# Kernel optimization log

Hardware: AMD Instinct MI355X
Metric: run time of the kernel (lower is better)

## Reference

```python
import jax, jax.numpy as jnp
import numpy as np

N = 100000      # nodes
E = 1600000     # edges
F_IN = 64       # node_features
F_OUT = 32      # output_size


def _cheb2(H, row, col, w_norm, theta, bias):
    # ChebConv K=2, sym normalization, lambda_max=2 (GCLSTM default):
    # L_hat = L - I = -D^{-1/2} A D^{-1/2}, so T0 = H, T1 = -A_norm H
    agg = jax.ops.segment_sum(w_norm[:, None] * H[col], row, num_segments=N)  # [N, F_OUT]
    return H @ theta[0] - agg @ theta[1] + bias


def setup_inputs() -> dict:
    key = jax.random.key(0)
    ks = jax.random.split(key, 24)
    inp = {}
    inp["x"] = jax.random.normal(ks[0], (N, F_IN), jnp.float32)
    inp["edge_index"] = jax.random.randint(ks[1], (2, E), 0, N)
    inp["edge_weight"] = jax.random.uniform(ks[2], (E,), jnp.float32)
    inp["h"] = jax.random.normal(ks[3], (N, F_OUT), jnp.float32)
    inp["c"] = jax.random.normal(ks[4], (N, F_OUT), jnp.float32)
    s_in = float(1.0 / np.sqrt(F_IN))
    s_out = float(1.0 / np.sqrt(F_OUT))
    i = 5
    for g in "ifco":
        inp[f"W_{g}"] = jax.random.uniform(ks[i], (F_IN, F_OUT), jnp.float32, -s_in, s_in); i += 1
        inp[f"b_{g}"] = jax.random.uniform(ks[i], (1, F_OUT), jnp.float32, -s_in, s_in); i += 1
        inp[f"theta_{g}"] = jax.random.uniform(ks[i], (2, F_OUT, F_OUT), jnp.float32, -s_out, s_out); i += 1
        inp[f"cb_{g}"] = jax.random.uniform(ks[i], (F_OUT,), jnp.float32, -s_out, s_out); i += 1
    inp["W_lin"] = jax.random.uniform(ks[i], (F_OUT, 1), jnp.float32, -s_out, s_out); i += 1
    inp["b_lin"] = jax.random.uniform(ks[i], (1,), jnp.float32, -s_out, s_out)
    return inp


def reference(x, edge_index, edge_weight, h, c,
              W_i, b_i, theta_i, cb_i,
              W_f, b_f, theta_f, cb_f,
              W_c, b_c, theta_c, cb_c,
              W_o, b_o, theta_o, cb_o,
              W_lin, b_lin):
    row, col = edge_index[0], edge_index[1]
    # symmetric normalization of edge weights (get_laplacian 'sym')
    deg = jax.ops.segment_sum(edge_weight, row, num_segments=N)
    dis = jnp.where(deg > 0, jax.lax.rsqrt(jnp.where(deg > 0, deg, 1.0)), 0.0)
    w_norm = dis[row] * edge_weight * dis[col]  # [E]
    # GCLSTM gates: input x through dense W, hidden h through ChebConv
    I = jax.nn.sigmoid(x @ W_i + _cheb2(h, row, col, w_norm, theta_i, cb_i) + b_i)
    Fg = jax.nn.sigmoid(x @ W_f + _cheb2(h, row, col, w_norm, theta_f, cb_f) + b_f)
    T = jnp.tanh(x @ W_c + _cheb2(h, row, col, w_norm, theta_c, cb_c) + b_c)
    C = Fg * c + I * T
    O = jax.nn.sigmoid(x @ W_o + _cheb2(h, row, col, w_norm, theta_o, cb_o) + b_o)
    H = O * jnp.tanh(C)
    # wrapper head: relu then Linear(out, 1)
    return jax.nn.relu(H) @ W_lin + b_lin  # [N, 1]
```

## Files before the change

### kernel.cpp

```cpp
#include <hip/hip_runtime.h>
#include <math.h>

#define NN 100000
#define NE 1600000
#define EPB 8192
#define NEB 196
#define NBUK 391
#define CAP 8192

#define DEGSCALE 16777216.0f

typedef __attribute__((ext_vector_type(8))) short bf16x8;
typedef __attribute__((ext_vector_type(4))) float f32x4;

#define MFMA(A, B, C) __builtin_amdgcn_mfma_f32_16x16x32_bf16(A, B, C, 0, 0, 0)

__device__ __forceinline__ float sigm(float z) { return 1.0f / (1.0f + expf(-z)); }

__device__ __forceinline__ void split1(float v, unsigned short* hi, unsigned short* lo) {
  unsigned u = __float_as_uint(v);
  *hi = (unsigned short)(u >> 16);
  float hf = __uint_as_float(u & 0xFFFF0000u);
  float lf = v - hf;
  *lo = (unsigned short)(__float_as_uint(lf) >> 16);
}

__device__ __forceinline__ void split8(const float* f, bf16x8* hi, bf16x8* lo) {
#pragma unroll
  for (int j = 0; j < 8; ++j) {
    unsigned short h, l;
    split1(f[j], &h, &l);
    (*hi)[j] = (short)h;
    (*lo)[j] = (short)l;
  }
}

__device__ __forceinline__ bf16x8 as_bf16x8(uint4 q) {
  union { uint4 q; bf16x8 v; } u;
  u.q = q;
  return u.v;
}

__device__ __forceinline__ void load8(const float4* p, int idx4, float* f) {
  float4 a = p[idx4];
  float4 b = p[idx4 + 1];
  f[0] = a.x; f[1] = a.y; f[2] = a.z; f[3] = a.w;
  f[4] = b.x; f[5] = b.y; f[6] = b.z; f[7] = b.w;
}


__global__ __launch_bounds__(256) void k_p1(const int* __restrict__ row,
                                            int* __restrict__ counts) {
  __shared__ int hist[NBUK];
  for (int i = threadIdx.x; i < NBUK; i += 256) hist[i] = 0;
  __syncthreads();
  int e0 = blockIdx.x * EPB;
  int e1 = min(e0 + EPB, NE);
  for (int e = e0 + (int)threadIdx.x; e < e1; e += 256)
    atomicAdd(&hist[row[e] >> 8], 1);
  __syncthreads();
  for (int i = threadIdx.x; i < NBUK; i += 256)
    counts[blockIdx.x * NBUK + i] = hist[i];
}

__global__ __launch_bounds__(256) void k_s1(int* __restrict__ counts,
                                            int* __restrict__ total) {
  __shared__ int s[256];
  int b = blockIdx.x;
  int t = threadIdx.x;
  int v = (t < NEB) ? counts[t * NBUK + b] : 0;
  s[t] = v;
  __syncthreads();
  for (int o = 1; o < 256; o <<= 1) {
    int a = (t >= o) ? s[t - o] : 0;
    __syncthreads();
    s[t] += a;
    __syncthreads();
  }
  if (t < NEB) counts[t * NBUK + b] = s[t] - v;
  if (t == 255) total[b] = s[255];
}

struct S2PParams {
  const int* total;
  int* bases;
  const float* W[4];
  const float* T0[4];
  const float* T1[4];
  const float* b[4];
  const float* cb[4];
  uint4* fh;
  uint4* fl;
  float* bias;
};

__global__ __launch_bounds__(512) void k_s2p(S2PParams pp) {
  if (blockIdx.x == 0) {
    __shared__ int s[512];
    int t = threadIdx.x;
    int v = (t < NBUK) ? pp.total[t] : 0;
    s[t] = v;
    __syncthreads();
    for (int o = 1; o < 512; o <<= 1) {
      int a = (t >= o) ? s[t - o] : 0;
      __syncthreads();
      s[t] += a;
      __syncthreads();
    }
    if (t < NBUK) pp.bases[t] = s[t] - v;
    if (t == 0) pp.bases[NBUK] = NE;
    return;
  }
  int idx = (blockIdx.x - 1) * 512 + threadIdx.x;
  if (idx < 2048) {
    int T = idx >> 6;
    int lane = idx & 63;
    int ncol = ((T & 7) * 16) + (lane & 15);
    int g = ncol >> 5;
    int c = ncol & 31;
    int kq = (lane >> 4) * 8;
    const float* mat;
    int kbase;
    if (T < 16) { mat = pp.W[g]; kbase = (T >> 3) * 32 + kq; }
    else if (T < 24) { mat = pp.T0[g]; kbase = kq; }
    else { mat = pp.T1[g]; kbase = kq; }
    unsigned hw[4], lw[4];
#pragma unroll
    for (int jj = 0; jj < 4; ++jj) {
      unsigned short h0, l0, h1, l1;
      split1(mat[(kbase + 2 * jj) * 32 + c], &h0, &l0);
      split1(mat[(kbase + 2 * jj + 1) * 32 + c], &h1, &l1);
      hw[jj] = (unsigned)h0 | ((unsigned)h1 << 16);
      lw[jj] = (unsigned)l0 | ((unsigned)l1 << 16);
    }
    pp.fh[idx] = make_uint4(hw[0], hw[1], hw[2], hw[3]);
    pp.fl[idx] = make_uint4(lw[0], lw[1], lw[2], lw[3]);
  }
  if (blockIdx.x == 1 && threadIdx.x < 128) {
    int g = threadIdx.x >> 5;
    int c = threadIdx.x & 31;
    pp.bias[threadIdx.x] = pp.b[g][c] + pp.cb[g][c];
  }
}

__global__ __launch_bounds__(256) void k_p2(const int* __restrict__ row,
                                            const int* __restrict__ col,
                                            const float* __restrict__ ew,
                                            const int* __restrict__ rel,
                                            const int* __restrict__ bases,
                                            int2* __restrict__ colw) {
  __shared__ int cursor[NBUK];
  for (int i = threadIdx.x; i < NBUK; i += 256)
    cursor[i] = bases[i] + rel[blockIdx.x * NBUK + i];
  __syncthreads();
  int e0 = blockIdx.x * EPB;
  int e1 = min(e0 + EPB, NE);
  for (int e = e0 + (int)threadIdx.x; e < e1; e += 256) {
    int r = row[e];
    int c = col[e];
    float w = ew[e];
    int slot = atomicAdd(&cursor[r >> 8], 1);
    colw[slot] = make_int2(c | ((r & 255) << 17), __float_as_int(w));
  }
}

__global__ __launch_bounds__(256) void k_bucket(const int* __restrict__ bases,
                                               int2* __restrict__ colw,
                                               int* __restrict__ rowptr,
                                               float* __restrict__ dis) {
  __shared__ int2 stage[CAP];
  __shared__ int cnt[256], degfx[256], s[256], cursor[256];
  int b = blockIdx.x;
  int base = bases[b];
  int M = bases[b + 1] - base;
  if (M > CAP) M = CAP;
  int t = threadIdx.x;
  cnt[t] = 0;
  degfx[t] = 0;
  __syncthreads();
  for (int i = t; i < M; i += 256) {
    int2 e = colw[base + i];
    stage[i] = e;
    int rl = (e.x >> 17) & 255;
    atomicAdd(&cnt[rl], 1);
    unsigned fx = (unsigned)(__int_as_float(e.y) * DEGSCALE + 0.5f);
    atomicAdd((unsigned*)&degfx[rl], fx);
  }
  __syncthreads();
  int v = cnt[t];
  s[t] = v;
  __syncthreads();
  for (int o = 1; o < 256; o <<= 1) {
    int a = (t >= o) ? s[t - o] : 0;
    __syncthreads();
    s[t] += a;
    __syncthreads();
  }
  int excl = s[t] - v;
  int node = b * 256 + t;
  if (node <= NN) rowptr[node] = base + excl;
  if (node < NN) {
    unsigned fx = (unsigned)degfx[t];
    dis[node] = fx ? rsqrtf((float)fx * (1.0f / DEGSCALE)) : 0.0f;
  }
  cursor[t] = excl;
  __syncthreads();
  for (int i = t; i < M; i += 256) {
    int2 e = stage[i];
    int rl = (e.x >> 17) & 255;
    int r = atomicAdd(&cursor[rl], 1);
    colw[base + r] = e;
  }
}

struct FusedParams {
  const float4* x4;
  const float4* h4;
  const float* cst;
  const int* rowptr;
  const int2* colw;
  const float* dis;
  const uint4* fh;
  const uint4* fl;
  const float* bias;
  const float* wlin;
  const float* blin;
  float* out;
};

__global__ __launch_bounds__(256) void k_fused(FusedParams p) {
  const int lane = threadIdx.x & 63;
  const int wv = threadIdx.x >> 6;
  const int m0 = blockIdx.x * 64 + wv * 16;
  const int mr = lane & 15;
  const int quad = lane >> 4;
  int m = m0 + mr;
  if (m >= NN) m = NN - 1;

  bf16x8 xh[2], xl[2], hh, hl, gh, gl;
  float f[8];
#pragma unroll
  for (int kt = 0; kt < 2; ++kt) {
    load8(p.x4, (m * 64 + kt * 32 + quad * 8) >> 2, f);
    split8(f, &xh[kt], &xl[kt]);
  }
  load8(p.h4, (m * 32 + quad * 8) >> 2, f);
  split8(f, &hh, &hl);

  float fa[8] = {0.f, 0.f, 0.f, 0.f, 0.f, 0.f, 0.f, 0.f};
  float fb[8] = {0.f, 0.f, 0.f, 0.f, 0.f, 0.f, 0.f, 0.f};
  {
    int s0 = p.rowptr[m];
    int s1v = p.rowptr[m + 1];
    int j = s0;
    for (; j + 1 < s1v; j += 2) {
      int2 cw0 = p.colw[j];
      int2 cw1 = p.colw[j + 1];
      int c0 = cw0.x & 0x1FFFF;
      int c1 = cw1.x & 0x1FFFF;
      float w0 = __int_as_float(cw0.y) * p.dis[c0];
      float w1 = __int_as_float(cw1.y) * p.dis[c1];
      const float4* hp0 = p.h4 + c0 * 8 + quad * 2;
      const float4* hp1 = p.h4 + c1 * 8 + quad * 2;
      float4 a0 = hp0[0], a1 = hp0[1];
      float4 b0 = hp1[0], b1 = hp1[1];
      fa[0] = fmaf(w0, a0.x, fa[0]); fa[1] = fmaf(w0, a0.y, fa[1]);
      fa[2] = fmaf(w0, a0.z, fa[2]); fa[3] = fmaf(w0, a0.w, fa[3]);
      fa[4] = fmaf(w0, a1.x, fa[4]); fa[5] = fmaf(w0, a1.y, fa[5]);
      fa[6] = fmaf(w0, a1.z, fa[6]); fa[7] = fmaf(w0, a1.w, fa[7]);
      fb[0] = fmaf(w1, b0.x, fb[0]); fb[1] = fmaf(w1, b0.y, fb[1]);
      fb[2] = fmaf(w1, b0.z, fb[2]); fb[3] = fmaf(w1, b0.w, fb[3]);
      fb[4] = fmaf(w1, b1.x, fb[4]); fb[5] = fmaf(w1, b1.y, fb[5]);
      fb[6] = fmaf(w1, b1.z, fb[6]); fb[7] = fmaf(w1, b1.w, fb[7]);
    }
    if (j < s1v) {
      int2 cw0 = p.colw[j];
      int c0 = cw0.x & 0x1FFFF;
      float w0 = __int_as_float(cw0.y) * p.dis[c0];
      const float4* hp0 = p.h4 + c0 * 8 + quad * 2;
      float4 a0 = hp0[0], a1 = hp0[1];
      fa[0] = fmaf(w0, a0.x, fa[0]); fa[1] = fmaf(w0, a0.y, fa[1]);
      fa[2] = fmaf(w0, a0.z, fa[2]); fa[3] = fmaf(w0, a0.w, fa[3]);
      fa[4] = fmaf(w0, a1.x, fa[4]); fa[5] = fmaf(w0, a1.y, fa[5]);
      fa[6] = fmaf(w0, a1.z, fa[6]); fa[7] = fmaf(w0, a1.w, fa[7]);
    }
  }
  {
    float dn = -p.dis[m];
#pragma unroll
    for (int j = 0; j < 8; ++j) f[j] = dn * (fa[j] + fb[j]);
    split8(f, &gh, &gl);
  }

  float wl0 = p.wlin[mr];
  float wl1 = p.wlin[mr + 16];
  float bl = p.blin[0];

  f32x4 acc[8];
#pragma unroll 2
  for (int nt = 0; nt < 8; ++nt) {
    float bv = p.bias[nt * 16 + mr];
    f32x4 a;
    a[0] = bv; a[1] = bv; a[2] = bv; a[3] = bv;
    bf16x8 b0h = as_bf16x8(p.fh[nt * 64 + lane]);
    bf16x8 b0l = as_bf16x8(p.fl[nt * 64 + lane]);
    bf16x8 b1h = as_bf16x8(p.fh[(8 + nt) * 64 + lane]);
    bf16x8 b1l = as_bf16x8(p.fl[(8 + nt) * 64 + lane]);
    bf16x8 t0h = as_bf16x8(p.fh[(16 + nt) * 64 + lane]);
    bf16x8 t0l = as_bf16x8(p.fl[(16 + nt) * 64 + lane]);
    bf16x8 t1h = as_bf16x8(p.fh[(24 + nt) * 64 + lane]);
    bf16x8 t1l = as_bf16x8(p.fl[(24 + nt) * 64 + lane]);
    a = MFMA(xh[0], b0h, a); a = MFMA(xh[0], b0l, a); a = MFMA(xl[0], b0h, a);
    a = MFMA(xh[1], b1h, a); a = MFMA(xh[1], b1l, a); a = MFMA(xl[1], b1h, a);
    a = MFMA(hh, t0h, a);    a = MFMA(hh, t0l, a);    a = MFMA(hl, t0h, a);
    a = MFMA(gh, t1h, a);    a = MFMA(gh, t1l, a);    a = MFMA(gl, t1h, a);
    acc[nt] = a;
  }

#pragma unroll
  for (int r = 0; r < 4; ++r) {
    int node = m0 + quad * 4 + r;
    int nc = node < NN ? node : NN - 1;
    float c0 = p.cst[nc * 32 + mr];
    float c1 = p.cst[nc * 32 + 16 + mr];
    float I0 = sigm(acc[0][r]), I1 = sigm(acc[1][r]);
    float F0 = sigm(acc[2][r]), F1 = sigm(acc[3][r]);
    float T0 = tanhf(acc[4][r]), T1 = tanhf(acc[5][r]);
    float O0 = sigm(acc[6][r]), O1 = sigm(acc[7][r]);
    float C0 = fmaf(F0, c0, I0 * T0);
    float C1 = fmaf(F1, c1, I1 * T1);
    float H0 = O0 * tanhf(C0);
    float H1 = O1 * tanhf(C1);
    float part = fmaf(fmaxf(H0, 0.f), wl0, fmaxf(H1, 0.f) * wl1);
#pragma unroll
    for (int s = 1; s < 16; s <<= 1) part += __shfl_xor(part, s, 64);
    if (mr == 0 && node < NN) p.out[node] = part + bl;
  }
}

extern "C" void kernel_launch(void* const* d_in, const int* in_sizes, int n_in,
                              void* d_out, int out_size, void* d_ws, size_t ws_size,
                              hipStream_t stream) {
  const float* x = (const float*)d_in[0];
  const int* row = (const int*)d_in[1];
  const int* col = row + NE;
  const float* ew = (const float*)d_in[2];
  const float* h = (const float*)d_in[3];
  const float* c = (const float*)d_in[4];

  float* ws = (float*)d_ws;
  float* dis = ws;
  int* rowptr = (int*)(ws + 100000);
  int* counts = (int*)(ws + 200004);
  int* total = (int*)(ws + 276640);
  int* bases = (int*)(ws + 277032);
  uint4* fh = (uint4*)(ws + 277424);
  uint4* fl = (uint4*)(ws + 285616);
  float* biasws = ws + 293808;
  int2* colw = (int2*)(ws + 293936);

  k_p1<<<NEB, 256, 0, stream>>>(row, counts);
  k_s1<<<NBUK, 256, 0, stream>>>(counts, total);

  S2PParams sp;
  sp.total = total;
  sp.bases = bases;
  for (int g = 0; g < 4; ++g) {
    sp.W[g] = (const float*)d_in[5 + 4 * g];
    sp.b[g] = (const float*)d_in[6 + 4 * g];
    sp.T0[g] = (const float*)d_in[7 + 4 * g];
    sp.T1[g] = sp.T0[g] + 1024;
    sp.cb[g] = (const float*)d_in[8 + 4 * g];
  }
  sp.fh = fh;
  sp.fl = fl;
  sp.bias = biasws;
  k_s2p<<<9, 512, 0, stream>>>(sp);

  k_p2<<<NEB, 256, 0, stream>>>(row, col, ew, counts, bases, colw);
  k_bucket<<<NBUK, 256, 0, stream>>>(bases, colw, rowptr, dis);

  FusedParams fp;
  fp.x4 = (const float4*)x;
  fp.h4 = (const float4*)h;
  fp.cst = c;
  fp.rowptr = rowptr;
  fp.colw = colw;
  fp.dis = dis;
  fp.fh = fh;
  fp.fl = fl;
  fp.bias = biasws;
  fp.wlin = (const float*)d_in[21];
  fp.blin = (const float*)d_in[22];
  fp.out = (float*)d_out;
  k_fused<<<(NN + 63) / 64, 256, 0, stream>>>(fp);
}
```

Measured before the change: 242.9 us.

## Replace bucketed CSR build with global-atomic counting sort and prescaled weights

The shared-memory two-level bucket sort (per-block histograms, scans, bucket scatter, in-bucket reorder) is replaced by a per-row counting sort. Row counts and degrees come from global atomics, followed by a two-kernel prefix scan and an atomic-cursor scatter that writes column/weight pairs. The scatter pre-multiplies each edge weight by dis[col], so the fused kernel no longer gathers dis per edge. The aggregation loop is also software-pipelined to load the next four edges early. The cost is heavy global atomic traffic on 100k counters, including float atomics that make the degree sum order nondeterministic, plus scattered uncoalesced writes; workspace regions for deg and btot are reused by colw.

Result: slower. 441.2 us (+81.6%).

```diff
diff --git a/kernel.cpp b/kernel.cpp
--- a/kernel.cpp
+++ b/kernel.cpp
@@ -3,12 +3,8 @@
 
 #define NN 100000
 #define NE 1600000
-#define EPB 8192
-#define NEB 196
 #define NBUK 391
-#define CAP 8192
-
-#define DEGSCALE 16777216.0f
+#define NPAD (NBUK * 256)
 
 typedef __attribute__((ext_vector_type(8))) short bf16x8;
 typedef __attribute__((ext_vector_type(4))) float f32x4;
@@ -49,41 +45,9 @@
 }
 
 
-__global__ __launch_bounds__(256) void k_p1(const int* __restrict__ row,
-                                            int* __restrict__ counts) {
-  __shared__ int hist[NBUK];
-  for (int i = threadIdx.x; i < NBUK; i += 256) hist[i] = 0;
-  __syncthreads();
-  int e0 = blockIdx.x * EPB;
-  int e1 = min(e0 + EPB, NE);
-  for (int e = e0 + (int)threadIdx.x; e < e1; e += 256)
-    atomicAdd(&hist[row[e] >> 8], 1);
-  __syncthreads();
-  for (int i = threadIdx.x; i < NBUK; i += 256)
-    counts[blockIdx.x * NBUK + i] = hist[i];
-}
-
-__global__ __launch_bounds__(256) void k_s1(int* __restrict__ counts,
-                                            int* __restrict__ total) {
-  __shared__ int s[256];
-  int b = blockIdx.x;
-  int t = threadIdx.x;
-  int v = (t < NEB) ? counts[t * NBUK + b] : 0;
-  s[t] = v;
-  __syncthreads();
-  for (int o = 1; o < 256; o <<= 1) {
-    int a = (t >= o) ? s[t - o] : 0;
-    __syncthreads();
-    s[t] += a;
-    __syncthreads();
-  }
-  if (t < NEB) counts[t * NBUK + b] = s[t] - v;
-  if (t == 255) total[b] = s[255];
-}
-
-struct S2PParams {
-  const int* total;
-  int* bases;
+struct InitParams {
+  int* cnt;
+  float* deg;
   const float* W[4];
   const float* T0[4];
   const float* T1[4];
@@ -94,24 +58,13 @@
   float* bias;
 };
 
-__global__ __launch_bounds__(512) void k_s2p(S2PParams pp) {
-  if (blockIdx.x == 0) {
-    __shared__ int s[512];
-    int t = threadIdx.x;
-    int v = (t < NBUK) ? pp.total[t] : 0;
-    s[t] = v;
-    __syncthreads();
-    for (int o = 1; o < 512; o <<= 1) {
-      int a = (t >= o) ? s[t - o] : 0;
-      __syncthreads();
-      s[t] += a;
-      __syncthreads();
-    }
-    if (t < NBUK) pp.bases[t] = s[t] - v;
-    if (t == 0) pp.bases[NBUK] = NE;
-    return;
-  }
-  int idx = (blockIdx.x - 1) * 512 + threadIdx.x;
+__global__ __launch_bounds__(512) void k_init(InitParams pp) {
+  int idx = blockIdx.x * 512 + threadIdx.x;
+  int stride = gridDim.x * 512;
+  for (int i = idx; i < NPAD; i += stride) {
+    pp.cnt[i] = 0;
+    pp.deg[i] = 0.0f;
+  }
   if (idx < 2048) {
     int T = idx >> 6;
     int lane = idx & 63;
@@ -136,58 +89,36 @@
     pp.fh[idx] = make_uint4(hw[0], hw[1], hw[2], hw[3]);
     pp.fl[idx] = make_uint4(lw[0], lw[1], lw[2], lw[3]);
   }
-  if (blockIdx.x == 1 && threadIdx.x < 128) {
-    int g = threadIdx.x >> 5;
-    int c = threadIdx.x & 31;
-    pp.bias[threadIdx.x] = pp.b[g][c] + pp.cb[g][c];
-  }
-}
-
-__global__ __launch_bounds__(256) void k_p2(const int* __restrict__ row,
-                                            const int* __restrict__ col,
-                                            const float* __restrict__ ew,
-                                            const int* __restrict__ rel,
-                                            const int* __restrict__ bases,
-                                            int2* __restrict__ colw) {
-  __shared__ int cursor[NBUK];
-  for (int i = threadIdx.x; i < NBUK; i += 256)
-    cursor[i] = bases[i] + rel[blockIdx.x * NBUK + i];
-  __syncthreads();
-  int e0 = blockIdx.x * EPB;
-  int e1 = min(e0 + EPB, NE);
-  for (int e = e0 + (int)threadIdx.x; e < e1; e += 256) {
+  if (idx < 128) {
+    int g = idx >> 5;
+    int c = idx & 31;
+    pp.bias[idx] = pp.b[g][c] + pp.cb[g][c];
+  }
+}
+
+__global__ __launch_bounds__(256) void k_hist(const int* __restrict__ row,
+                                              const float* __restrict__ ew,
+                                              int* __restrict__ cnt,
+                                              float* __restrict__ deg) {
+  int stride = gridDim.x * 256;
+  for (int e = blockIdx.x * 256 + threadIdx.x; e < NE; e += stride) {
     int r = row[e];
-    int c = col[e];
-    float w = ew[e];
-    int slot = atomicAdd(&cursor[r >> 8], 1);
-    colw[slot] = make_int2(c | ((r & 255) << 17), __float_as_int(w));
-  }
-}
-
-__global__ __launch_bounds__(256) void k_bucket(const int* __restrict__ bases,
-                                               int2* __restrict__ colw,
-                                               int* __restrict__ rowptr,
-                                               float* __restrict__ dis) {
-  __shared__ int2 stage[CAP];
-  __shared__ int cnt[256], degfx[256], s[256], cursor[256];
+    atomicAdd(&cnt[r], 1);
+    atomicAdd(&deg[r], ew[e]);
+  }
+}
+
+__global__ __launch_bounds__(256) void k_scan_a(const float* __restrict__ deg,
+                                                float* __restrict__ dis,
+                                                int* __restrict__ cursor,
+                                                int* __restrict__ btot) {
+  __shared__ int s[256];
   int b = blockIdx.x;
-  int base = bases[b];
-  int M = bases[b + 1] - base;
-  if (M > CAP) M = CAP;
   int t = threadIdx.x;
-  cnt[t] = 0;
-  degfx[t] = 0;
-  __syncthreads();
-  for (int i = t; i < M; i += 256) {
-    int2 e = colw[base + i];
-    stage[i] = e;
-    int rl = (e.x >> 17) & 255;
-    atomicAdd(&cnt[rl], 1);
-    unsigned fx = (unsigned)(__int_as_float(e.y) * DEGSCALE + 0.5f);
-    atomicAdd((unsigned*)&degfx[rl], fx);
-  }
-  __syncthreads();
-  int v = cnt[t];
+  int n = b * 256 + t;
+  int v = cursor[n];
+  float dg = deg[n];
+  if (n < NN) dis[n] = dg > 0.0f ? rsqrtf(dg) : 0.0f;
   s[t] = v;
   __syncthreads();
   for (int o = 1; o < 256; o <<= 1) {
@@ -196,20 +127,39 @@
     s[t] += a;
     __syncthreads();
   }
-  int excl = s[t] - v;
-  int node = b * 256 + t;
-  if (node <= NN) rowptr[node] = base + excl;
-  if (node < NN) {
-    unsigned fx = (unsigned)degfx[t];
-    dis[node] = fx ? rsqrtf((float)fx * (1.0f / DEGSCALE)) : 0.0f;
-  }
-  cursor[t] = excl;
+  cursor[n] = s[t] - v;
+  if (t == 255) btot[b] = s[255];
+}
+
+__global__ __launch_bounds__(256) void k_scan_c(const int* __restrict__ btot,
+                                                int* __restrict__ cursor) {
+  __shared__ int s[256];
+  int b = blockIdx.x;
+  int t = threadIdx.x;
+  int acc = 0;
+  for (int j = t; j < b; j += 256) acc += btot[j];
+  s[t] = acc;
   __syncthreads();
-  for (int i = t; i < M; i += 256) {
-    int2 e = stage[i];
-    int rl = (e.x >> 17) & 255;
-    int r = atomicAdd(&cursor[rl], 1);
-    colw[base + r] = e;
+  for (int o = 128; o > 0; o >>= 1) {
+    if (t < o) s[t] += s[t + o];
+    __syncthreads();
+  }
+  cursor[b * 256 + t] += s[0];
+}
+
+__global__ __launch_bounds__(256) void k_scatter(const int* __restrict__ row,
+                                                 const int* __restrict__ col,
+                                                 const float* __restrict__ ew,
+                                                 const float* __restrict__ dis,
+                                                 int* __restrict__ cursor,
+                                                 int2* __restrict__ colw) {
+  int stride = gridDim.x * 256;
+  for (int e = blockIdx.x * 256 + threadIdx.x; e < NE; e += stride) {
+    int r = row[e];
+    int c = col[e];
+    float w = ew[e] * dis[c];
+    int slot = atomicAdd(&cursor[r], 1);
+    colw[slot] = make_int2(c, __float_as_int(w));
   }
 }
 
@@ -217,7 +167,7 @@
   const float4* x4;
   const float4* h4;
   const float* cst;
-  const int* rowptr;
+  const int* cursor;
   const int2* colw;
   const float* dis;
   const uint4* fh;
@@ -228,6 +178,17 @@
   float* out;
 };
 
+__device__ __forceinline__ void accrow(const FusedParams& p, int quad, int2 cw,
+                                       float* acc) {
+  const float4* hp = p.h4 + (cw.x * 8 + quad * 2);
+  float4 a0 = hp[0], a1 = hp[1];
+  float w = __int_as_float(cw.y);
+  acc[0] = fmaf(w, a0.x, acc[0]); acc[1] = fmaf(w, a0.y, acc[1]);
+  acc[2] = fmaf(w, a0.z, acc[2]); acc[3] = fmaf(w, a0.w, acc[3]);
+  acc[4] = fmaf(w, a1.x, acc[4]); acc[5] = fmaf(w, a1.y, acc[5]);
+  acc[6] = fmaf(w, a1.z, acc[6]); acc[7] = fmaf(w, a1.w, acc[7]);
+}
+
 __global__ __launch_bounds__(256) void k_fused(FusedParams p) {
   const int lane = threadIdx.x & 63;
   const int wv = threadIdx.x >> 6;
@@ -250,40 +211,48 @@
   float fa[8] = {0.f, 0.f, 0.f, 0.f, 0.f, 0.f, 0.f, 0.f};
   float fb[8] = {0.f, 0.f, 0.f, 0.f, 0.f, 0.f, 0.f, 0.f};
   {
-    int s0 = p.rowptr[m];
-    int s1v = p.rowptr[m + 1];
-    int j = s0;
-    for (; j + 1 < s1v; j += 2) {
-      int2 cw0 = p.colw[j];
-      int2 cw1 = p.colw[j + 1];
-      int c0 = cw0.x & 0x1FFFF;
-      int c1 = cw1.x & 0x1FFFF;
-      float w0 = __int_as_float(cw0.y) * p.dis[c0];
-      float w1 = __int_as_float(cw1.y) * p.dis[c1];
-      const float4* hp0 = p.h4 + c0 * 8 + quad * 2;
-      const float4* hp1 = p.h4 + c1 * 8 + quad * 2;
-      float4 a0 = hp0[0], a1 = hp0[1];
-      float4 b0 = hp1[0], b1 = hp1[1];
-      fa[0] = fmaf(w0, a0.x, fa[0]); fa[1] = fmaf(w0, a0.y, fa[1]);
-      fa[2] = fmaf(w0, a0.z, fa[2]); fa[3] = fmaf(w0, a0.w, fa[3]);
-      fa[4] = fmaf(w0, a1.x, fa[4]); fa[5] = fmaf(w0, a1.y, fa[5]);
-      fa[6] = fmaf(w0, a1.z, fa[6]); fa[7] = fmaf(w0, a1.w, fa[7]);
-      fb[0] = fmaf(w1, b0.x, fb[0]); fb[1] = fmaf(w1, b0.y, fb[1]);
-      fb[2] = fmaf(w1, b0.z, fb[2]); fb[3] = fmaf(w1, b0.w, fb[3]);
-      fb[4] = fmaf(w1, b1.x, fb[4]); fb[5] = fmaf(w1, b1.y, fb[5]);
-      fb[6] = fmaf(w1, b1.z, fb[6]); fb[7] = fmaf(w1, b1.w, fb[7]);
+    int end = p.cursor[m];
+    int s0 = (m == 0) ? 0 : p.cursor[m - 1];
+    int rem = end - s0;
+    const int2* ep = p.colw + s0;
+    int i = 0;
+    if (rem >= 4) {
+      int2 w0 = ep[0], w1 = ep[1], w2 = ep[2], w3 = ep[3];
+      for (i = 4; i + 3 < rem; i += 4) {
+        const float4* h0 = p.h4 + (w0.x * 8 + quad * 2);
+        const float4* h1 = p.h4 + (w1.x * 8 + quad * 2);
+        const float4* h2 = p.h4 + (w2.x * 8 + quad * 2);
+        const float4* h3 = p.h4 + (w3.x * 8 + quad * 2);
+        float4 a0 = h0[0], a1 = h0[1];
+        float4 b0 = h1[0], b1 = h1[1];
+        float4 c0 = h2[0], c1 = h2[1];
+        float4 d0 = h3[0], d1 = h3[1];
+        float f0 = __int_as_float(w0.y), f1 = __int_as_float(w1.y);
+        float f2 = __int_as_float(w2.y), f3 = __int_as_float(w3.y);
+        w0 = ep[i]; w1 = ep[i + 1]; w2 = ep[i + 2]; w3 = ep[i + 3];
+        fa[0] = fmaf(f0, a0.x, fa[0]); fa[1] = fmaf(f0, a0.y, fa[1]);
+        fa[2] = fmaf(f0, a0.z, fa[2]); fa[3] = fmaf(f0, a0.w, fa[3]);
+        fa[4] = fmaf(f0, a1.x, fa[4]); fa[5] = fmaf(f0, a1.y, fa[5]);
+        fa[6] = fmaf(f0, a1.z, fa[6]); fa[7] = fmaf(f0, a1.w, fa[7]);
+        fb[0] = fmaf(f1, b0.x, fb[0]); fb[1] = fmaf(f1, b0.y, fb[1]);
+        fb[2] = fmaf(f1, b0.z, fb[2]); fb[3] = fmaf(f1, b0.w, fb[3]);
+        fb[4] = fmaf(f1, b1.x, fb[4]); fb[5] = fmaf(f1, b1.y, fb[5]);
+        fb[6] = fmaf(f1, b1.z, fb[6]); fb[7] = fmaf(f1, b1.w, fb[7]);
+        fa[0] = fmaf(f2, c0.x, fa[0]); fa[1] = fmaf(f2, c0.y, fa[1]);
+        fa[2] = fmaf(f2, c0.z, fa[2]); fa[3] = fmaf(f2, c0.w, fa[3]);
+        fa[4] = fmaf(f2, c1.x, fa[4]); fa[5] = fmaf(f2, c1.y, fa[5]);
+        fa[6] = fmaf(f2, c1.z, fa[6]); fa[7] = fmaf(f2, c1.w, fa[7]);
+        fb[0] = fmaf(f3, d0.x, fb[0]); fb[1] = fmaf(f3, d0.y, fb[1]);
+        fb[2] = fmaf(f3, d0.z, fb[2]); fb[3] = fmaf(f3, d0.w, fb[3]);
+        fb[4] = fmaf(f3, d1.x, fb[4]); fb[5] = fmaf(f3, d1.y, fb[5]);
+        fb[6] = fmaf(f3, d1.z, fb[6]); fb[7] = fmaf(f3, d1.w, fb[7]);
+      }
+      accrow(p, quad, w0, fa);
+      accrow(p, quad, w1, fb);
+      accrow(p, quad, w2, fa);
+      accrow(p, quad, w3, fb);
     }
-    if (j < s1v) {
-      int2 cw0 = p.colw[j];
-      int c0 = cw0.x & 0x1FFFF;
-      float w0 = __int_as_float(cw0.y) * p.dis[c0];
-      const float4* hp0 = p.h4 + c0 * 8 + quad * 2;
-      float4 a0 = hp0[0], a1 = hp0[1];
-      fa[0] = fmaf(w0, a0.x, fa[0]); fa[1] = fmaf(w0, a0.y, fa[1]);
-      fa[2] = fmaf(w0, a0.z, fa[2]); fa[3] = fmaf(w0, a0.w, fa[3]);
-      fa[4] = fmaf(w0, a1.x, fa[4]); fa[5] = fmaf(w0, a1.y, fa[5]);
-      fa[6] = fmaf(w0, a1.z, fa[6]); fa[7] = fmaf(w0, a1.w, fa[7]);
-    }
+    for (; i < rem; ++i) accrow(p, quad, ep[i], fa);
   }
   {
     float dn = -p.dis[m];
@@ -350,41 +319,39 @@
 
   float* ws = (float*)d_ws;
   float* dis = ws;
-  int* rowptr = (int*)(ws + 100000);
-  int* counts = (int*)(ws + 200004);
-  int* total = (int*)(ws + 276640);
-  int* bases = (int*)(ws + 277032);
-  uint4* fh = (uint4*)(ws + 277424);
-  uint4* fl = (uint4*)(ws + 285616);
-  float* biasws = ws + 293808;
-  int2* colw = (int2*)(ws + 293936);
-
-  k_p1<<<NEB, 256, 0, stream>>>(row, counts);
-  k_s1<<<NBUK, 256, 0, stream>>>(counts, total);
-
-  S2PParams sp;
-  sp.total = total;
-  sp.bases = bases;
+  int* cursor = (int*)(ws + 100000);
+  uint4* fh = (uint4*)(ws + 200096);
+  uint4* fl = (uint4*)(ws + 208288);
+  float* biasws = ws + 216480;
+  float* deg = ws + 216608;
+  int* btot = (int*)(ws + 316704);
+  int2* colw = (int2*)(ws + 216608);
+
+  InitParams ip;
+  ip.cnt = cursor;
+  ip.deg = deg;
   for (int g = 0; g < 4; ++g) {
-    sp.W[g] = (const float*)d_in[5 + 4 * g];
-    sp.b[g] = (const float*)d_in[6 + 4 * g];
-    sp.T0[g] = (const float*)d_in[7 + 4 * g];
-    sp.T1[g] = sp.T0[g] + 1024;
-    sp.cb[g] = (const float*)d_in[8 + 4 * g];
-  }
-  sp.fh = fh;
-  sp.fl = fl;
-  sp.bias = biasws;
-  k_s2p<<<9, 512, 0, stream>>>(sp);
-
-  k_p2<<<NEB, 256, 0, stream>>>(row, col, ew, counts, bases, colw);
-  k_bucket<<<NBUK, 256, 0, stream>>>(bases, colw, rowptr, dis);
+    ip.W[g] = (const float*)d_in[5 + 4 * g];
+    ip.b[g] = (const float*)d_in[6 + 4 * g];
+    ip.T0[g] = (const float*)d_in[7 + 4 * g];
+    ip.T1[g] = ip.T0[g] + 1024;
+    ip.cb[g] = (const float*)d_in[8 + 4 * g];
+  }
+  ip.fh = fh;
+  ip.fl = fl;
+  ip.bias = biasws;
+  k_init<<<98, 512, 0, stream>>>(ip);
+
+  k_hist<<<2048, 256, 0, stream>>>(row, ew, cursor, deg);
+  k_scan_a<<<NBUK, 256, 0, stream>>>(deg, dis, cursor, btot);
+  k_scan_c<<<NBUK, 256, 0, stream>>>(btot, cursor);
+  k_scatter<<<2048, 256, 0, stream>>>(row, col, ew, dis, cursor, colw);
 
   FusedParams fp;
   fp.x4 = (const float4*)x;
   fp.h4 = (const float4*)h;
   fp.cst = c;
-  fp.rowptr = rowptr;
+  fp.cursor = cursor;
   fp.colw = colw;
   fp.dis = dis;
   fp.fh = fh;
```

## Replace per-row CSR sort with 128-node buckets and shared-memory atomic aggregation

Applied to the files above, without the earlier changes.

Drops the second-level per-row sort (k_bucket) and builds only 128-node buckets. Degrees are computed with float shared atomics, and the fused kernel scatters neighbor features into a shared 128x33 accumulator with atomics before the MFMA gate stage. The intent is to remove the staging and re-sort pass and the rowptr build. The cost is 32 LDS atomics per edge, non-deterministic float summation order, and only 782 blocks in the fused kernel.

New measurement: 527.3 us. 117% more time.

```diff
diff --git a/kernel.cpp b/kernel.cpp
--- a/kernel.cpp
+++ b/kernel.cpp
@@ -3,12 +3,11 @@
 
 #define NN 100000
 #define NE 1600000
+#define BSH 7
+#define BMSK 127
+#define NBUK 782
 #define EPB 8192
 #define NEB 196
-#define NBUK 391
-#define CAP 8192
-
-#define DEGSCALE 16777216.0f
 
 typedef __attribute__((ext_vector_type(8))) short bf16x8;
 typedef __attribute__((ext_vector_type(4))) float f32x4;
@@ -57,7 +56,7 @@
   int e0 = blockIdx.x * EPB;
   int e1 = min(e0 + EPB, NE);
   for (int e = e0 + (int)threadIdx.x; e < e1; e += 256)
-    atomicAdd(&hist[row[e] >> 8], 1);
+    atomicAdd(&hist[row[e] >> BSH], 1);
   __syncthreads();
   for (int i = threadIdx.x; i < NBUK; i += 256)
     counts[blockIdx.x * NBUK + i] = hist[i];
@@ -94,14 +93,14 @@
   float* bias;
 };
 
-__global__ __launch_bounds__(512) void k_s2p(S2PParams pp) {
+__global__ __launch_bounds__(1024) void k_s2p(S2PParams pp) {
+  int t = threadIdx.x;
   if (blockIdx.x == 0) {
-    __shared__ int s[512];
-    int t = threadIdx.x;
+    __shared__ int s[1024];
     int v = (t < NBUK) ? pp.total[t] : 0;
     s[t] = v;
     __syncthreads();
-    for (int o = 1; o < 512; o <<= 1) {
+    for (int o = 1; o < 1024; o <<= 1) {
       int a = (t >= o) ? s[t - o] : 0;
       __syncthreads();
       s[t] += a;
@@ -109,9 +108,13 @@
     }
     if (t < NBUK) pp.bases[t] = s[t] - v;
     if (t == 0) pp.bases[NBUK] = NE;
+    if (t >= 896) {
+      int i = t - 896;
+      pp.bias[i] = pp.b[i >> 5][i & 31] + pp.cb[i >> 5][i & 31];
+    }
     return;
   }
-  int idx = (blockIdx.x - 1) * 512 + threadIdx.x;
+  int idx = (blockIdx.x - 1) * 1024 + t;
   if (idx < 2048) {
     int T = idx >> 6;
     int lane = idx & 63;
@@ -136,11 +139,6 @@
     pp.fh[idx] = make_uint4(hw[0], hw[1], hw[2], hw[3]);
     pp.fl[idx] = make_uint4(lw[0], lw[1], lw[2], lw[3]);
   }
-  if (blockIdx.x == 1 && threadIdx.x < 128) {
-    int g = threadIdx.x >> 5;
-    int c = threadIdx.x & 31;
-    pp.bias[threadIdx.x] = pp.b[g][c] + pp.cb[g][c];
-  }
 }
 
 __global__ __launch_bounds__(256) void k_p2(const int* __restrict__ row,
@@ -159,57 +157,30 @@
     int r = row[e];
     int c = col[e];
     float w = ew[e];
-    int slot = atomicAdd(&cursor[r >> 8], 1);
-    colw[slot] = make_int2(c | ((r & 255) << 17), __float_as_int(w));
-  }
-}
-
-__global__ __launch_bounds__(256) void k_bucket(const int* __restrict__ bases,
-                                               int2* __restrict__ colw,
-                                               int* __restrict__ rowptr,
-                                               float* __restrict__ dis) {
-  __shared__ int2 stage[CAP];
-  __shared__ int cnt[256], degfx[256], s[256], cursor[256];
+    int slot = atomicAdd(&cursor[r >> BSH], 1);
+    colw[slot] = make_int2(c | ((r & BMSK) << 17), __float_as_int(w));
+  }
+}
+
+__global__ __launch_bounds__(256) void k_deg(const int* __restrict__ bases,
+                                             const int2* __restrict__ colw,
+                                             float* __restrict__ dis) {
+  __shared__ float dg[128];
   int b = blockIdx.x;
+  int t = threadIdx.x;
+  if (t < 128) dg[t] = 0.0f;
+  __syncthreads();
   int base = bases[b];
   int M = bases[b + 1] - base;
-  if (M > CAP) M = CAP;
-  int t = threadIdx.x;
-  cnt[t] = 0;
-  degfx[t] = 0;
-  __syncthreads();
   for (int i = t; i < M; i += 256) {
     int2 e = colw[base + i];
-    stage[i] = e;
-    int rl = (e.x >> 17) & 255;
-    atomicAdd(&cnt[rl], 1);
-    unsigned fx = (unsigned)(__int_as_float(e.y) * DEGSCALE + 0.5f);
-    atomicAdd((unsigned*)&degfx[rl], fx);
-  }
-  __syncthreads();
-  int v = cnt[t];
-  s[t] = v;
-  __syncthreads();
-  for (int o = 1; o < 256; o <<= 1) {
-    int a = (t >= o) ? s[t - o] : 0;
-    __syncthreads();
-    s[t] += a;
-    __syncthreads();
-  }
-  int excl = s[t] - v;
-  int node = b * 256 + t;
-  if (node <= NN) rowptr[node] = base + excl;
-  if (node < NN) {
-    unsigned fx = (unsigned)degfx[t];
-    dis[node] = fx ? rsqrtf((float)fx * (1.0f / DEGSCALE)) : 0.0f;
-  }
-  cursor[t] = excl;
-  __syncthreads();
-  for (int i = t; i < M; i += 256) {
-    int2 e = stage[i];
-    int rl = (e.x >> 17) & 255;
-    int r = atomicAdd(&cursor[rl], 1);
-    colw[base + r] = e;
+    atomicAdd(&dg[e.x >> 17], __int_as_float(e.y));
+  }
+  __syncthreads();
+  int node = (b << BSH) + t;
+  if (t < 128 && node < NN) {
+    float d = dg[t];
+    dis[node] = d > 0.0f ? rsqrtf(d) : 0.0f;
   }
 }
 
@@ -217,7 +188,7 @@
   const float4* x4;
   const float4* h4;
   const float* cst;
-  const int* rowptr;
+  const int* bases;
   const int2* colw;
   const float* dis;
   const uint4* fh;
@@ -229,112 +200,115 @@
 };
 
 __global__ __launch_bounds__(256) void k_fused(FusedParams p) {
-  const int lane = threadIdx.x & 63;
-  const int wv = threadIdx.x >> 6;
-  const int m0 = blockIdx.x * 64 + wv * 16;
+  __shared__ float agg[128 * 33];
+  const int t = threadIdx.x;
+  const int b = blockIdx.x;
+  const int bbase = b << BSH;
+  for (int i = t; i < 128 * 33; i += 256) agg[i] = 0.0f;
+  __syncthreads();
+
+  {
+    int base = p.bases[b];
+    int M = p.bases[b + 1] - base;
+    for (int i = t; i < M; i += 256) {
+      int2 e = p.colw[base + i];
+      int c = e.x & 0x1FFFF;
+      float w = __int_as_float(e.y) * p.dis[c];
+      float* ag = &agg[(e.x >> 17) * 33];
+      const float4* hp = p.h4 + c * 8;
+      float4 q0 = hp[0], q1 = hp[1], q2 = hp[2], q3 = hp[3];
+      float4 q4 = hp[4], q5 = hp[5], q6 = hp[6], q7 = hp[7];
+      atomicAdd(&ag[0],  w * q0.x); atomicAdd(&ag[1],  w * q0.y);
+      atomicAdd(&ag[2],  w * q0.z); atomicAdd(&ag[3],  w * q0.w);
+      atomicAdd(&ag[4],  w * q1.x); atomicAdd(&ag[5],  w * q1.y);
+      atomicAdd(&ag[6],  w * q1.z); atomicAdd(&ag[7],  w * q1.w);
+      atomicAdd(&ag[8],  w * q2.x); atomicAdd(&ag[9],  w * q2.y);
+      atomicAdd(&ag[10], w * q2.z); atomicAdd(&ag[11], w * q2.w);
+      atomicAdd(&ag[12], w * q3.x); atomicAdd(&ag[13], w * q3.y);
+      atomicAdd(&ag[14], w * q3.z); atomicAdd(&ag[15], w * q3.w);
+      atomicAdd(&ag[16], w * q4.x); atomicAdd(&ag[17], w * q4.y);
+      atomicAdd(&ag[18], w * q4.z); atomicAdd(&ag[19], w * q4.w);
+      atomicAdd(&ag[20], w * q5.x); atomicAdd(&ag[21], w * q5.y);
+      atomicAdd(&ag[22], w * q5.z); atomicAdd(&ag[23], w * q5.w);
+      atomicAdd(&ag[24], w * q6.x); atomicAdd(&ag[25], w * q6.y);
+      atomicAdd(&ag[26], w * q6.z); atomicAdd(&ag[27], w * q6.w);
+      atomicAdd(&ag[28], w * q7.x); atomicAdd(&ag[29], w * q7.y);
+      atomicAdd(&ag[30], w * q7.z); atomicAdd(&ag[31], w * q7.w);
+    }
+  }
+  __syncthreads();
+
+  const int lane = t & 63;
+  const int wv = t >> 6;
   const int mr = lane & 15;
   const int quad = lane >> 4;
-  int m = m0 + mr;
-  if (m >= NN) m = NN - 1;
-
-  bf16x8 xh[2], xl[2], hh, hl, gh, gl;
-  float f[8];
-#pragma unroll
-  for (int kt = 0; kt < 2; ++kt) {
-    load8(p.x4, (m * 64 + kt * 32 + quad * 8) >> 2, f);
-    split8(f, &xh[kt], &xl[kt]);
-  }
-  load8(p.h4, (m * 32 + quad * 8) >> 2, f);
-  split8(f, &hh, &hl);
-
-  float fa[8] = {0.f, 0.f, 0.f, 0.f, 0.f, 0.f, 0.f, 0.f};
-  float fb[8] = {0.f, 0.f, 0.f, 0.f, 0.f, 0.f, 0.f, 0.f};
-  {
-    int s0 = p.rowptr[m];
-    int s1v = p.rowptr[m + 1];
-    int j = s0;
-    for (; j + 1 < s1v; j += 2) {
-      int2 cw0 = p.colw[j];
-      int2 cw1 = p.colw[j + 1];
-      int c0 = cw0.x & 0x1FFFF;
-      int c1 = cw1.x & 0x1FFFF;
-      float w0 = __int_as_float(cw0.y) * p.dis[c0];
-      float w1 = __int_as_float(cw1.y) * p.dis[c1];
-      const float4* hp0 = p.h4 + c0 * 8 + quad * 2;
-      const float4* hp1 = p.h4 + c1 * 8 + quad * 2;
-      float4 a0 = hp0[0], a1 = hp0[1];
-      float4 b0 = hp1[0], b1 = hp1[1];
-      fa[0] = fmaf(w0, a0.x, fa[0]); fa[1] = fmaf(w0, a0.y, fa[1]);
-      fa[2] = fmaf(w0, a0.z, fa[2]); fa[3] = fmaf(w0, a0.w, fa[3]);
-      fa[4] = fmaf(w0, a1.x, fa[4]); fa[5] = fmaf(w0, a1.y, fa[5]);
-      fa[6] = fmaf(w0, a1.z, fa[6]); fa[7] = fmaf(w0, a1.w, fa[7]);
-      fb[0] = fmaf(w1, b0.x, fb[0]); fb[1] = fmaf(w1, b0.y, fb[1]);
-      fb[2] = fmaf(w1, b0.z, fb[2]); fb[3] = fmaf(w1, b0.w, fb[3]);
-      fb[4] = fmaf(w1, b1.x, fb[4]); fb[5] = fmaf(w1, b1.y, fb[5]);
-      fb[6] = fmaf(w1, b1.z, fb[6]); fb[7] = fmaf(w1, b1.w, fb[7]);
-    }
-    if (j < s1v) {
-      int2 cw0 = p.colw[j];
-      int c0 = cw0.x & 0x1FFFF;
-      float w0 = __int_as_float(cw0.y) * p.dis[c0];
-      const float4* hp0 = p.h4 + c0 * 8 + quad * 2;
-      float4 a0 = hp0[0], a1 = hp0[1];
-      fa[0] = fmaf(w0, a0.x, fa[0]); fa[1] = fmaf(w0, a0.y, fa[1]);
-      fa[2] = fmaf(w0, a0.z, fa[2]); fa[3] = fmaf(w0, a0.w, fa[3]);
-      fa[4] = fmaf(w0, a1.x, fa[4]); fa[5] = fmaf(w0, a1.y, fa[5]);
-      fa[6] = fmaf(w0, a1.z, fa[6]); fa[7] = fmaf(w0, a1.w, fa[7]);
-    }
-  }
-  {
-    float dn = -p.dis[m];
-#pragma unroll
-    for (int j = 0; j < 8; ++j) f[j] = dn * (fa[j] + fb[j]);
-    split8(f, &gh, &gl);
-  }
-
   float wl0 = p.wlin[mr];
   float wl1 = p.wlin[mr + 16];
   float bl = p.blin[0];
 
-  f32x4 acc[8];
+  for (int grp = 0; grp < 2; ++grp) {
+    const int m0 = bbase + (wv + 4 * grp) * 16;
+    int m = m0 + mr;
+    if (m >= NN) m = NN - 1;
+
+    bf16x8 xh[2], xl[2], hh, hl, gh, gl;
+    float f[8];
+#pragma unroll
+    for (int kt = 0; kt < 2; ++kt) {
+      load8(p.x4, (m * 64 + kt * 32 + quad * 8) >> 2, f);
+      split8(f, &xh[kt], &xl[kt]);
+    }
+    load8(p.h4, (m * 32 + quad * 8) >> 2, f);
+    split8(f, &hh, &hl);
+    {
+      int rlm = m - bbase;
+      float dn = -p.dis[m];
+      const float* ag = &agg[rlm * 33 + quad * 8];
+#pragma unroll
+      for (int j = 0; j < 8; ++j) f[j] = dn * ag[j];
+      split8(f, &gh, &gl);
+    }
+
+    f32x4 acc[8];
 #pragma unroll 2
-  for (int nt = 0; nt < 8; ++nt) {
-    float bv = p.bias[nt * 16 + mr];
-    f32x4 a;
-    a[0] = bv; a[1] = bv; a[2] = bv; a[3] = bv;
-    bf16x8 b0h = as_bf16x8(p.fh[nt * 64 + lane]);
-    bf16x8 b0l = as_bf16x8(p.fl[nt * 64 + lane]);
-    bf16x8 b1h = as_bf16x8(p.fh[(8 + nt) * 64 + lane]);
-    bf16x8 b1l = as_bf16x8(p.fl[(8 + nt) * 64 + lane]);
-    bf16x8 t0h = as_bf16x8(p.fh[(16 + nt) * 64 + lane]);
-    bf16x8 t0l = as_bf16x8(p.fl[(16 + nt) * 64 + lane]);
-    bf16x8 t1h = as_bf16x8(p.fh[(24 + nt) * 64 + lane]);
-    bf16x8 t1l = as_bf16x8(p.fl[(24 + nt) * 64 + lane]);
-    a = MFMA(xh[0], b0h, a); a = MFMA(xh[0], b0l, a); a = MFMA(xl[0], b0h, a);
-    a = MFMA(xh[1], b1h, a); a = MFMA(xh[1], b1l, a); a = MFMA(xl[1], b1h, a);
-    a = MFMA(hh, t0h, a);    a = MFMA(hh, t0l, a);    a = MFMA(hl, t0h, a);
-    a = MFMA(gh, t1h, a);    a = MFMA(gh, t1l, a);    a = MFMA(gl, t1h, a);
-    acc[nt] = a;
-  }
-
-#pragma unroll
-  for (int r = 0; r < 4; ++r) {
-    int node = m0 + quad * 4 + r;
-    int nc = node < NN ? node : NN - 1;
-    float c0 = p.cst[nc * 32 + mr];
-    float c1 = p.cst[nc * 32 + 16 + mr];
-    float I0 = sigm(acc[0][r]), I1 = sigm(acc[1][r]);
-    float F0 = sigm(acc[2][r]), F1 = sigm(acc[3][r]);
-    float T0 = tanhf(acc[4][r]), T1 = tanhf(acc[5][r]);
-    float O0 = sigm(acc[6][r]), O1 = sigm(acc[7][r]);
-    float C0 = fmaf(F0, c0, I0 * T0);
-    float C1 = fmaf(F1, c1, I1 * T1);
-    float H0 = O0 * tanhf(C0);
-    float H1 = O1 * tanhf(C1);
-    float part = fmaf(fmaxf(H0, 0.f), wl0, fmaxf(H1, 0.f) * wl1);
-#pragma unroll
-    for (int s = 1; s < 16; s <<= 1) part += __shfl_xor(part, s, 64);
-    if (mr == 0 && node < NN) p.out[node] = part + bl;
+    for (int nt = 0; nt < 8; ++nt) {
+      float bv = p.bias[nt * 16 + mr];
+      f32x4 a;
+      a[0] = bv; a[1] = bv; a[2] = bv; a[3] = bv;
+      bf16x8 b0h = as_bf16x8(p.fh[nt * 64 + lane]);
+      bf16x8 b0l = as_bf16x8(p.fl[nt * 64 + lane]);
+      bf16x8 b1h = as_bf16x8(p.fh[(8 + nt) * 64 + lane]);
+      bf16x8 b1l = as_bf16x8(p.fl[(8 + nt) * 64 + lane]);
+      bf16x8 t0h = as_bf16x8(p.fh[(16 + nt) * 64 + lane]);
+      bf16x8 t0l = as_bf16x8(p.fl[(16 + nt) * 64 + lane]);
+      bf16x8 t1h = as_bf16x8(p.fh[(24 + nt) * 64 + lane]);
+      bf16x8 t1l = as_bf16x8(p.fl[(24 + nt) * 64 + lane]);
+      a = MFMA(xh[0], b0h, a); a = MFMA(xh[0], b0l, a); a = MFMA(xl[0], b0h, a);
+      a = MFMA(xh[1], b1h, a); a = MFMA(xh[1], b1l, a); a = MFMA(xl[1], b1h, a);
+      a = MFMA(hh, t0h, a);    a = MFMA(hh, t0l, a);    a = MFMA(hl, t0h, a);
+      a = MFMA(gh, t1h, a);    a = MFMA(gh, t1l, a);    a = MFMA(gl, t1h, a);
+      acc[nt] = a;
+    }
+
+#pragma unroll
+    for (int r = 0; r < 4; ++r) {
+      int node = m0 + quad * 4 + r;
+      int nc = node < NN ? node : NN - 1;
+      float c0 = p.cst[nc * 32 + mr];
+      float c1 = p.cst[nc * 32 + 16 + mr];
+      float I0 = sigm(acc[0][r]), I1 = sigm(acc[1][r]);
+      float F0 = sigm(acc[2][r]), F1 = sigm(acc[3][r]);
+      float T0 = tanhf(acc[4][r]), T1 = tanhf(acc[5][r]);
+      float O0 = sigm(acc[6][r]), O1 = sigm(acc[7][r]);
+      float C0 = fmaf(F0, c0, I0 * T0);
+      float C1 = fmaf(F1, c1, I1 * T1);
+      float H0 = O0 * tanhf(C0);
+      float H1 = O1 * tanhf(C1);
+      float part = fmaf(fmaxf(H0, 0.f), wl0, fmaxf(H1, 0.f) * wl1);
+#pragma unroll
+      for (int s = 1; s < 16; s <<= 1) part += __shfl_xor(part, s, 64);
+      if (mr == 0 && node < NN) p.out[node] = part + bl;
+    }
   }
 }
 
@@ -350,14 +324,13 @@
 
   float* ws = (float*)d_ws;
   float* dis = ws;
-  int* rowptr = (int*)(ws + 100000);
-  int* counts = (int*)(ws + 200004);
-  int* total = (int*)(ws + 276640);
-  int* bases = (int*)(ws + 277032);
-  uint4* fh = (uint4*)(ws + 277424);
-  uint4* fl = (uint4*)(ws + 285616);
-  float* biasws = ws + 293808;
-  int2* colw = (int2*)(ws + 293936);
+  int* total = (int*)(ws + 100000);
+  int* bases = (int*)(ws + 100784);
+  int* counts = (int*)(ws + 101568);
+  uint4* fh = (uint4*)(ws + 254840);
+  uint4* fl = (uint4*)(ws + 263032);
+  float* biasws = ws + 271224;
+  int2* colw = (int2*)(ws + 271352);
 
   k_p1<<<NEB, 256, 0, stream>>>(row, counts);
   k_s1<<<NBUK, 256, 0, stream>>>(counts, total);
@@ -375,16 +348,16 @@
   sp.fh = fh;
   sp.fl = fl;
   sp.bias = biasws;
-  k_s2p<<<9, 512, 0, stream>>>(sp);
+  k_s2p<<<3, 1024, 0, stream>>>(sp);
 
   k_p2<<<NEB, 256, 0, stream>>>(row, col, ew, counts, bases, colw);
-  k_bucket<<<NBUK, 256, 0, stream>>>(bases, colw, rowptr, dis);
+  k_deg<<<NBUK, 256, 0, stream>>>(bases, colw, dis);
 
   FusedParams fp;
   fp.x4 = (const float4*)x;
   fp.h4 = (const float4*)h;
   fp.cst = c;
-  fp.rowptr = rowptr;
+  fp.bases = bases;
   fp.colw = colw;
   fp.dis = dis;
   fp.fh = fh;
@@ -393,5 +366,5 @@
   fp.wlin = (const float*)d_in[21];
   fp.blin = (const float*)d_in[22];
   fp.out = (float*)d_out;
-  k_fused<<<(NN + 63) / 64, 256, 0, stream>>>(fp);
-}
+  k_fused<<<NBUK, 256, 0, stream>>>(fp);
+}
```
